# Performance work log

Hardware: AMD Instinct MI355X
Metric: run time of the kernel (lower is better)

The kernel has to match this reference:

```python
import jax, jax.numpy as jnp
import numpy as np

EMBED_DIM = 1024
NUM_HEADS = 16
HEAD_DIM = EMBED_DIM // NUM_HEADS

def setup_inputs() -> dict:
    key = jax.random.key(0)
    k1, k2, k3 = jax.random.split(key, 3)
    x = jax.random.normal(k1, (4, 2048, EMBED_DIM), dtype=jnp.float32)
    # Linear weights stored as [out, in] like torch; we apply x @ W.T
    W_qkv = jax.random.normal(k2, (3 * EMBED_DIM, EMBED_DIM), dtype=jnp.float32) * (EMBED_DIM ** -0.5)
    W_proj = jax.random.normal(k3, (EMBED_DIM, EMBED_DIM), dtype=jnp.float32) * (EMBED_DIM ** -0.5)
    return {"x": x, "W_qkv": W_qkv, "W_proj": W_proj}

def reference(x, W_qkv, W_proj):
    B, T, C = x.shape
    H, D = NUM_HEADS, HEAD_DIM
    qkv = x @ W_qkv.T                          # [B,T,3C]
    q, k, v = jnp.split(qkv, 3, axis=-1)
    q = q.reshape(B, T, H, D).transpose(0, 2, 1, 3)  # [B,H,T,D]
    k = k.reshape(B, T, H, D).transpose(0, 2, 1, 3)
    v = v.reshape(B, T, H, D).transpose(0, 2, 1, 3)
    scores = jnp.einsum('bhqd,bhkd->bhqk', q, k) / jnp.sqrt(jnp.asarray(D, x.dtype))
    causal = jnp.tril(jnp.ones((T, T), dtype=bool))
    scores = jnp.where(causal, scores, -jnp.inf)
    weights = jax.nn.softmax(scores, axis=-1)
    out = jnp.einsum('bhqk,bhkd->bhqd', weights, v)  # [B,H,T,D]
    out = out.transpose(0, 2, 1, 3).reshape(B, T, C)
    return out @ W_proj.T
```

## Files before the change

kernel.cpp:

```cpp
#include <hip/hip_runtime.h>

#define T_SEQ 2048
#define NB 4
#define NH 16
#define HD 64
#define CDIM 1024
#define MROWS (NB * T_SEQ)

typedef __attribute__((ext_vector_type(8))) short short8;
typedef __attribute__((ext_vector_type(4))) float floatx4;

static __device__ __forceinline__ unsigned short f2bf(float f) {
  union { float f; unsigned int i; } c; c.f = f;
  return (unsigned short)((c.i + 0x7FFFu + ((c.i >> 16) & 1u)) >> 16);
}
static __device__ __forceinline__ unsigned short f2bf_trunc(float f) {
  union { float f; unsigned int i; } c; c.f = f;
  return (unsigned short)(c.i >> 16);
}

static __device__ __forceinline__ void gl2lds16(const void* g, void* l) {
  __builtin_amdgcn_global_load_lds(
      (const __attribute__((address_space(1))) unsigned int*)g,
      (__attribute__((address_space(3))) unsigned int*)l, 16, 0, 0);
}

#define X4 (MROWS * CDIM / 4)
#define WQ4 (3 * CDIM * CDIM / 4)
#define WP4 (CDIM * CDIM / 4)
__global__ __launch_bounds__(256) void cast3_bf16(const float* __restrict__ x,
                                                  const float* __restrict__ wq,
                                                  const float* __restrict__ wp,
                                                  unsigned short* __restrict__ out) {
  const int i = blockIdx.x * 256 + threadIdx.x;
  const float* src; int off;
  if (i < X4) { src = x; off = i; }
  else if (i < X4 + WQ4) { src = wq; off = i - X4; }
  else { src = wp; off = i - X4 - WQ4; }
  const float4 v = ((const float4*)src)[off];
  ushort4 o;
  o.x = f2bf(v.x); o.y = f2bf(v.y); o.z = f2bf(v.z); o.w = f2bf(v.w);
  ((ushort4*)out)[i] = o;
}

#define Q_PRESCALE 0.18033688f

__global__ __launch_bounds__(256) void gemm_bf16_qkv(
    const unsigned short* __restrict__ A,
    const unsigned short* __restrict__ B,
    unsigned short* __restrict__ Oq,
    unsigned short* __restrict__ Ok,
    unsigned short* __restrict__ Ovt,
    const int K)
{
  __shared__ unsigned short As[128 * 32];
  __shared__ unsigned short Bs[128 * 32];
  const int tid = threadIdx.x;
  const int w = tid >> 6, l = tid & 63;
  const int quad = l >> 4, l15 = l & 15;
  const int m0 = blockIdx.y * 128, n0 = blockIdx.x * 128;
  const int wm = (w >> 1) * 64, wn = (w & 1) * 64;
  const int srow = l >> 2;
  const int scol = ((l & 3) ^ (srow & 3)) * 8;

  floatx4 acc[4][4];
#pragma unroll
  for (int mi = 0; mi < 4; ++mi)
#pragma unroll
    for (int ni = 0; ni < 4; ++ni) acc[mi][ni] = (floatx4){0.f, 0.f, 0.f, 0.f};

  const unsigned short* Ag = A + (size_t)(m0 + w * 32 + srow) * K + scol;
  const unsigned short* Bg = B + (size_t)(n0 + w * 32 + srow) * K + scol;
  unsigned short* Al0 = &As[(w * 32) * 32];
  unsigned short* Al1 = &As[(w * 32 + 16) * 32];
  unsigned short* Bl0 = &Bs[(w * 32) * 32];
  unsigned short* Bl1 = &Bs[(w * 32 + 16) * 32];
  const int sq = quad ^ (l15 & 3);

  for (int k0 = 0; k0 < K; k0 += 32) {
    __syncthreads();
    gl2lds16(Ag + k0, Al0);
    gl2lds16(Ag + (size_t)16 * K + k0, Al1);
    gl2lds16(Bg + k0, Bl0);
    gl2lds16(Bg + (size_t)16 * K + k0, Bl1);
    __syncthreads();
    short8 af[4], bfr[4];
#pragma unroll
    for (int mi = 0; mi < 4; ++mi)
      af[mi] = *(const short8*)&As[(wm + mi * 16 + l15) * 32 + sq * 8];
#pragma unroll
    for (int ni = 0; ni < 4; ++ni)
      bfr[ni] = *(const short8*)&Bs[(wn + ni * 16 + l15) * 32 + sq * 8];
#pragma unroll
    for (int mi = 0; mi < 4; ++mi)
#pragma unroll
      for (int ni = 0; ni < 4; ++ni)
        acc[mi][ni] = __builtin_amdgcn_mfma_f32_16x16x32_bf16(af[mi], bfr[ni], acc[mi][ni], 0, 0, 0);
  }

  const int mbase = m0 + wm + quad * 4;
#pragma unroll
  for (int ni = 0; ni < 4; ++ni) {
    const int n = n0 + wn + ni * 16 + l15;
    const int which = n >> 10;
    const int h = (n >> 6) & (NH - 1), d = n & (HD - 1);
    if (which == 2) {
#pragma unroll
      for (int mi = 0; mi < 4; ++mi) {
        const int m = mbase + mi * 16;
        const int b = m >> 11, t0 = m & (T_SEQ - 1);
        ushort4 pk;
        pk.x = f2bf(acc[mi][ni][0]); pk.y = f2bf(acc[mi][ni][1]);
        pk.z = f2bf(acc[mi][ni][2]); pk.w = f2bf(acc[mi][ni][3]);
        *(ushort4*)(Ovt + ((size_t)((b * NH + h) * HD + d) << 11) + t0) = pk;
      }
    } else {
      unsigned short* dst = (which == 0) ? Oq : Ok;
      const float sc = (which == 0) ? Q_PRESCALE : 1.0f;
#pragma unroll
      for (int mi = 0; mi < 4; ++mi)
#pragma unroll
        for (int r = 0; r < 4; ++r) {
          const int m = mbase + mi * 16 + r;
          const int b = m >> 11, t = m & (T_SEQ - 1);
          dst[(((size_t)(b * NH + h) * T_SEQ + t) << 6) + d] = f2bf(acc[mi][ni][r] * sc);
        }
    }
  }
}

__global__ __launch_bounds__(256) void gemm_bf16_proj(
    const unsigned short* __restrict__ A,
    const unsigned short* __restrict__ B,
    float* __restrict__ O,
    const int N, const int K)
{
  __shared__ unsigned short As[128 * 32];
  __shared__ unsigned short Bs[128 * 32];
  const int tid = threadIdx.x;
  const int w = tid >> 6, l = tid & 63;
  const int quad = l >> 4, l15 = l & 15;
  const int m0 = blockIdx.y * 128, n0 = blockIdx.x * 128;
  const int wm = (w >> 1) * 64, wn = (w & 1) * 64;
  const int srow = l >> 2;
  const int scol = ((l & 3) ^ (srow & 3)) * 8;

  floatx4 acc[4][4];
#pragma unroll
  for (int mi = 0; mi < 4; ++mi)
#pragma unroll
    for (int ni = 0; ni < 4; ++ni) acc[mi][ni] = (floatx4){0.f, 0.f, 0.f, 0.f};

  const unsigned short* Ag = A + (size_t)(m0 + w * 32 + srow) * K + scol;
  const unsigned short* Bg = B + (size_t)(n0 + w * 32 + srow) * K + scol;
  unsigned short* Al0 = &As[(w * 32) * 32];
  unsigned short* Al1 = &As[(w * 32 + 16) * 32];
  unsigned short* Bl0 = &Bs[(w * 32) * 32];
  unsigned short* Bl1 = &Bs[(w * 32 + 16) * 32];
  const int sq = quad ^ (l15 & 3);

  for (int k0 = 0; k0 < K; k0 += 32) {
    __syncthreads();
    gl2lds16(Ag + k0, Al0);
    gl2lds16(Ag + (size_t)16 * K + k0, Al1);
    gl2lds16(Bg + k0, Bl0);
    gl2lds16(Bg + (size_t)16 * K + k0, Bl1);
    __syncthreads();
    short8 af[4], bfr[4];
#pragma unroll
    for (int mi = 0; mi < 4; ++mi)
      af[mi] = *(const short8*)&As[(wm + mi * 16 + l15) * 32 + sq * 8];
#pragma unroll
    for (int ni = 0; ni < 4; ++ni)
      bfr[ni] = *(const short8*)&Bs[(wn + ni * 16 + l15) * 32 + sq * 8];
#pragma unroll
    for (int mi = 0; mi < 4; ++mi)
#pragma unroll
      for (int ni = 0; ni < 4; ++ni)
        acc[mi][ni] = __builtin_amdgcn_mfma_f32_16x16x32_bf16(af[mi], bfr[ni], acc[mi][ni], 0, 0, 0);
  }

#pragma unroll
  for (int mi = 0; mi < 4; ++mi)
#pragma unroll
    for (int r = 0; r < 4; ++r) {
      const int m = m0 + wm + mi * 16 + quad * 4 + r;
#pragma unroll
      for (int ni = 0; ni < 4; ++ni)
        O[(size_t)m * N + n0 + wn + ni * 16 + l15] = acc[mi][ni][r];
    }
}

#define TK 64

__global__ __launch_bounds__(512) void attn_mfma(
    const unsigned short* __restrict__ Q,
    const unsigned short* __restrict__ K,
    const unsigned short* __restrict__ Vt,
    unsigned short* __restrict__ O)
{
  __shared__ unsigned short Ks[TK * HD];
  __shared__ unsigned short Vts[HD * TK];
  __shared__ unsigned short Pw[8][16 * 68];
  const int tid = threadIdx.x;
  const int w = tid >> 6, l = tid & 63;
  const int quad = l >> 4, l15 = l & 15;
  const int drow = 8 * w + (l >> 3);
  const int dch = ((l & 7) ^ (l >> 3)) * 8;
  const int sw7 = l15 & 7;

  const int bh = blockIdx.x & 63;
  const int pp = blockIdx.x >> 6;
  const int b = bh >> 4, h = bh & 15;
  const size_t hoff = (size_t)bh * T_SEQ * HD;
  const unsigned short* Qh = Q + hoff;
  const unsigned short* Kdma = K + hoff + (size_t)drow * HD + dch;
  const unsigned short* Vdma = Vt + hoff + ((size_t)drow << 11) + dch;
  unsigned short* KsW = &Ks[w * 512];
  unsigned short* VtsW = &Vts[w * 512];

  short8 ones;
#pragma unroll
  for (int j = 0; j < 8; ++j) ones[j] = (short)0x3F80;

#pragma unroll 1
  for (int ii = 0; ii < 2; ++ii) {
    const int qtile = ii ? pp : (15 - pp);
    const int qw = qtile * 128 + w * 16;

    short8 qf[2];
    {
      const int qrow = qw + l15;
      qf[0] = *(const short8*)(Qh + (size_t)qrow * HD + quad * 8);
      qf[1] = *(const short8*)(Qh + (size_t)qrow * HD + 32 + quad * 8);
    }

    floatx4 Of[4];
#pragma unroll
    for (int dc = 0; dc < 4; ++dc) Of[dc] = (floatx4){0.f, 0.f, 0.f, 0.f};
    floatx4 lacc = (floatx4){0.f, 0.f, 0.f, 0.f};

    const int nkt = 2 * qtile + 2;
    for (int kt = 0; kt < nkt; ++kt) {
      const int kt0 = kt * TK;
      __syncthreads();
      gl2lds16(Kdma + (size_t)kt0 * HD, KsW);
      gl2lds16(Vdma + kt0, VtsW);
      __syncthreads();

      if (qw + 15 >= kt0) {
        floatx4 Sf[4];
#pragma unroll
        for (int cb = 0; cb < 4; ++cb) {
          Sf[cb] = (floatx4){0.f, 0.f, 0.f, 0.f};
          const int krow = cb * 16 + l15;
#pragma unroll
          for (int h2 = 0; h2 < 2; ++h2) {
            const int ch = (h2 * 4 + quad) ^ sw7;
            const short8 kf = *(const short8*)&Ks[krow * 64 + ch * 8];
            Sf[cb] = __builtin_amdgcn_mfma_f32_16x16x32_bf16(qf[h2], kf, Sf[cb], 0, 0, 0);
          }
        }
        const bool full = (kt0 + 63 <= qw);
        if (full) {
#pragma unroll
          for (int cb = 0; cb < 4; ++cb)
#pragma unroll
            for (int r = 0; r < 4; ++r)
              Pw[w][(quad * 4 + r) * 68 + cb * 16 + l15] = f2bf_trunc(exp2f(Sf[cb][r]));
        } else {
#pragma unroll
          for (int cb = 0; cb < 4; ++cb) {
            const int key = kt0 + cb * 16 + l15;
#pragma unroll
            for (int r = 0; r < 4; ++r) {
              const int qrow = qw + quad * 4 + r;
              const float p = (key > qrow) ? 0.f : exp2f(Sf[cb][r]);
              Pw[w][(quad * 4 + r) * 68 + cb * 16 + l15] = f2bf_trunc(p);
            }
          }
        }
#pragma unroll
        for (int kg = 0; kg < 2; ++kg) {
          const short8 pf = *(const short8*)&Pw[w][l15 * 68 + kg * 32 + quad * 8];
          lacc = __builtin_amdgcn_mfma_f32_16x16x32_bf16(pf, ones, lacc, 0, 0, 0);
#pragma unroll
          for (int dc = 0; dc < 4; ++dc) {
            const int vrow = dc * 16 + l15;
            const int ch = (kg * 4 + quad) ^ sw7;
            const short8 vf = *(const short8*)&Vts[vrow * 64 + ch * 8];
            Of[dc] = __builtin_amdgcn_mfma_f32_16x16x32_bf16(pf, vf, Of[dc], 0, 0, 0);
          }
        }
      }
    }

#pragma unroll
    for (int r = 0; r < 4; ++r) {
      const float inv = 1.f / lacc[r];
      const int q = qw + quad * 4 + r;
#pragma unroll
      for (int dc = 0; dc < 4; ++dc)
        O[(size_t)(b * T_SEQ + q) * CDIM + h * HD + dc * 16 + l15] = f2bf(Of[dc][r] * inv);
    }
  }
}

extern "C" void kernel_launch(void* const* d_in, const int* in_sizes, int n_in,
                              void* d_out, int out_size, void* d_ws, size_t ws_size,
                              hipStream_t stream) {
  const float* x     = (const float*)d_in[0];
  const float* Wqkv  = (const float*)d_in[1];
  const float* Wproj = (const float*)d_in[2];
  float* out = (float*)d_out;

  const size_t XSZ = (size_t)MROWS * CDIM;
  const size_t WQSZ = (size_t)3 * CDIM * CDIM;
  const size_t WPSZ = (size_t)CDIM * CDIM;
  unsigned short* xb  = (unsigned short*)d_ws;
  unsigned short* wqb = xb + XSZ;
  unsigned short* wpb = wqb + WQSZ;
  unsigned short* qbuf = wpb + WPSZ;
  unsigned short* kbuf = qbuf + XSZ;
  unsigned short* vtbuf = kbuf + XSZ;
  unsigned short* abuf = vtbuf + XSZ;

  cast3_bf16<<<(X4 + WQ4 + WP4) / 256, 256, 0, stream>>>(x, Wqkv, Wproj, xb);

  dim3 g1(3 * CDIM / 128, MROWS / 128);
  gemm_bf16_qkv<<<g1, 256, 0, stream>>>(xb, wqb, qbuf, kbuf, vtbuf, CDIM);

  attn_mfma<<<512, 512, 0, stream>>>(qbuf, kbuf, vtbuf, abuf);

  dim3 g3(CDIM / 128, MROWS / 128);
  gemm_bf16_proj<<<g3, 256, 0, stream>>>(abuf, wpb, out, CDIM, CDIM);
}
```

Before: 266.7 us.

## Double-buffer LDS tiles and transpose MFMA outputs for vectorized stores

All three kernels now double-buffer their LDS tiles. The next K or V tile is issued with global_load_lds before the current one is consumed, which drops one barrier per iteration and overlaps loads with MFMA work. MFMA operands are swapped so each lane's accumulator holds consecutive output columns. That allows packed ushort4/float4 stores for Q, K, attention output and projection output, and a transposed P layout in attention. The cost is twice the LDS per block, which may lower occupancy. The V-transpose store also becomes a scalar scatter.

```diff
diff --git a/kernel.cpp b/kernel.cpp
--- a/kernel.cpp
+++ b/kernel.cpp
@@ -53,8 +53,8 @@
     unsigned short* __restrict__ Ovt,
     const int K)
 {
-  __shared__ unsigned short As[128 * 32];
-  __shared__ unsigned short Bs[128 * 32];
+  __shared__ unsigned short As[2][128 * 32];
+  __shared__ unsigned short Bs[2][128 * 32];
   const int tid = threadIdx.x;
   const int w = tid >> 6, l = tid & 63;
   const int quad = l >> 4, l15 = l & 15;
@@ -71,60 +71,70 @@
 
   const unsigned short* Ag = A + (size_t)(m0 + w * 32 + srow) * K + scol;
   const unsigned short* Bg = B + (size_t)(n0 + w * 32 + srow) * K + scol;
-  unsigned short* Al0 = &As[(w * 32) * 32];
-  unsigned short* Al1 = &As[(w * 32 + 16) * 32];
-  unsigned short* Bl0 = &Bs[(w * 32) * 32];
-  unsigned short* Bl1 = &Bs[(w * 32 + 16) * 32];
+  const int d0 = (w * 32) * 32, d1 = (w * 32 + 16) * 32;
   const int sq = quad ^ (l15 & 3);
 
+  gl2lds16(Ag, &As[0][d0]);
+  gl2lds16(Ag + (size_t)16 * K, &As[0][d1]);
+  gl2lds16(Bg, &Bs[0][d0]);
+  gl2lds16(Bg + (size_t)16 * K, &Bs[0][d1]);
+
   for (int k0 = 0; k0 < K; k0 += 32) {
+    const int cur = (k0 >> 5) & 1, nxt = 1 - cur;
     __syncthreads();
-    gl2lds16(Ag + k0, Al0);
-    gl2lds16(Ag + (size_t)16 * K + k0, Al1);
-    gl2lds16(Bg + k0, Bl0);
-    gl2lds16(Bg + (size_t)16 * K + k0, Bl1);
-    __syncthreads();
+    if (k0 + 32 < K) {
+      gl2lds16(Ag + k0 + 32, &As[nxt][d0]);
+      gl2lds16(Ag + (size_t)16 * K + k0 + 32, &As[nxt][d1]);
+      gl2lds16(Bg + k0 + 32, &Bs[nxt][d0]);
+      gl2lds16(Bg + (size_t)16 * K + k0 + 32, &Bs[nxt][d1]);
+    }
     short8 af[4], bfr[4];
 #pragma unroll
     for (int mi = 0; mi < 4; ++mi)
-      af[mi] = *(const short8*)&As[(wm + mi * 16 + l15) * 32 + sq * 8];
+      af[mi] = *(const short8*)&As[cur][(wm + mi * 16 + l15) * 32 + sq * 8];
 #pragma unroll
     for (int ni = 0; ni < 4; ++ni)
-      bfr[ni] = *(const short8*)&Bs[(wn + ni * 16 + l15) * 32 + sq * 8];
+      bfr[ni] = *(const short8*)&Bs[cur][(wn + ni * 16 + l15) * 32 + sq * 8];
 #pragma unroll
     for (int mi = 0; mi < 4; ++mi)
 #pragma unroll
       for (int ni = 0; ni < 4; ++ni)
-        acc[mi][ni] = __builtin_amdgcn_mfma_f32_16x16x32_bf16(af[mi], bfr[ni], acc[mi][ni], 0, 0, 0);
-  }
-
-  const int mbase = m0 + wm + quad * 4;
-#pragma unroll
-  for (int ni = 0; ni < 4; ++ni) {
-    const int n = n0 + wn + ni * 16 + l15;
-    const int which = n >> 10;
-    const int h = (n >> 6) & (NH - 1), d = n & (HD - 1);
-    if (which == 2) {
+        acc[mi][ni] = __builtin_amdgcn_mfma_f32_16x16x32_bf16(bfr[ni], af[mi], acc[mi][ni], 0, 0, 0);
+  }
+
+  const int which = n0 >> 10;
+  if (which < 2) {
+    unsigned short* dst = (which == 0) ? Oq : Ok;
+    const float sc = (which == 0) ? Q_PRESCALE : 1.0f;
+#pragma unroll
+    for (int ni = 0; ni < 4; ++ni) {
+      const int n = n0 + wn + ni * 16 + quad * 4;
+      const int h = (n >> 6) & (NH - 1), d = n & (HD - 1);
 #pragma unroll
       for (int mi = 0; mi < 4; ++mi) {
-        const int m = mbase + mi * 16;
-        const int b = m >> 11, t0 = m & (T_SEQ - 1);
+        const int m = m0 + wm + mi * 16 + l15;
+        const int b = m >> 11, t = m & (T_SEQ - 1);
         ushort4 pk;
-        pk.x = f2bf(acc[mi][ni][0]); pk.y = f2bf(acc[mi][ni][1]);
-        pk.z = f2bf(acc[mi][ni][2]); pk.w = f2bf(acc[mi][ni][3]);
-        *(ushort4*)(Ovt + ((size_t)((b * NH + h) * HD + d) << 11) + t0) = pk;
+        pk.x = f2bf(acc[mi][ni][0] * sc); pk.y = f2bf(acc[mi][ni][1] * sc);
+        pk.z = f2bf(acc[mi][ni][2] * sc); pk.w = f2bf(acc[mi][ni][3] * sc);
+        *(ushort4*)(dst + (((size_t)(b * NH + h) * T_SEQ + t) << 6) + d) = pk;
       }
-    } else {
-      unsigned short* dst = (which == 0) ? Oq : Ok;
-      const float sc = (which == 0) ? Q_PRESCALE : 1.0f;
-#pragma unroll
-      for (int mi = 0; mi < 4; ++mi)
+    }
+  } else {
+#pragma unroll
+    for (int ni = 0; ni < 4; ++ni) {
+      const int nb = n0 + wn + ni * 16 + quad * 4;
+      const int h = (nb >> 6) & (NH - 1);
+#pragma unroll
+      for (int mi = 0; mi < 4; ++mi) {
+        const int m = m0 + wm + mi * 16 + l15;
+        const int b = m >> 11, t = m & (T_SEQ - 1);
 #pragma unroll
         for (int r = 0; r < 4; ++r) {
-          const int m = mbase + mi * 16 + r;
-          const int b = m >> 11, t = m & (T_SEQ - 1);
-          dst[(((size_t)(b * NH + h) * T_SEQ + t) << 6) + d] = f2bf(acc[mi][ni][r] * sc);
+          const int d = (nb + r) & (HD - 1);
+          Ovt[((size_t)((b * NH + h) * HD + d) << 11) + t] = f2bf(acc[mi][ni][r]);
         }
+      }
     }
   }
 }
@@ -135,8 +145,8 @@
     float* __restrict__ O,
     const int N, const int K)
 {
-  __shared__ unsigned short As[128 * 32];
-  __shared__ unsigned short Bs[128 * 32];
+  __shared__ unsigned short As[2][128 * 32];
+  __shared__ unsigned short Bs[2][128 * 32];
   const int tid = threadIdx.x;
   const int w = tid >> 6, l = tid & 63;
   const int quad = l >> 4, l15 = l & 15;
@@ -153,45 +163,51 @@
 
   const unsigned short* Ag = A + (size_t)(m0 + w * 32 + srow) * K + scol;
   const unsigned short* Bg = B + (size_t)(n0 + w * 32 + srow) * K + scol;
-  unsigned short* Al0 = &As[(w * 32) * 32];
-  unsigned short* Al1 = &As[(w * 32 + 16) * 32];
-  unsigned short* Bl0 = &Bs[(w * 32) * 32];
-  unsigned short* Bl1 = &Bs[(w * 32 + 16) * 32];
+  const int d0 = (w * 32) * 32, d1 = (w * 32 + 16) * 32;
   const int sq = quad ^ (l15 & 3);
 
+  gl2lds16(Ag, &As[0][d0]);
+  gl2lds16(Ag + (size_t)16 * K, &As[0][d1]);
+  gl2lds16(Bg, &Bs[0][d0]);
+  gl2lds16(Bg + (size_t)16 * K, &Bs[0][d1]);
+
   for (int k0 = 0; k0 < K; k0 += 32) {
+    const int cur = (k0 >> 5) & 1, nxt = 1 - cur;
     __syncthreads();
-    gl2lds16(Ag + k0, Al0);
-    gl2lds16(Ag + (size_t)16 * K + k0, Al1);
-    gl2lds16(Bg + k0, Bl0);
-    gl2lds16(Bg + (size_t)16 * K + k0, Bl1);
-    __syncthreads();
+    if (k0 + 32 < K) {
+      gl2lds16(Ag + k0 + 32, &As[nxt][d0]);
+      gl2lds16(Ag + (size_t)16 * K + k0 + 32, &As[nxt][d1]);
+      gl2lds16(Bg + k0 + 32, &Bs[nxt][d0]);
+      gl2lds16(Bg + (size_t)16 * K + k0 + 32, &Bs[nxt][d1]);
+    }
     short8 af[4], bfr[4];
 #pragma unroll
     for (int mi = 0; mi < 4; ++mi)
-      af[mi] = *(const short8*)&As[(wm + mi * 16 + l15) * 32 + sq * 8];
+      af[mi] = *(const short8*)&As[cur][(wm + mi * 16 + l15) * 32 + sq * 8];
 #pragma unroll
     for (int ni = 0; ni < 4; ++ni)
-      bfr[ni] = *(const short8*)&Bs[(wn + ni * 16 + l15) * 32 + sq * 8];
+      bfr[ni] = *(const short8*)&Bs[cur][(wn + ni * 16 + l15) * 32 + sq * 8];
 #pragma unroll
     for (int mi = 0; mi < 4; ++mi)
 #pragma unroll
       for (int ni = 0; ni < 4; ++ni)
-        acc[mi][ni] = __builtin_amdgcn_mfma_f32_16x16x32_bf16(af[mi], bfr[ni], acc[mi][ni], 0, 0, 0);
-  }
-
-#pragma unroll
-  for (int mi = 0; mi < 4; ++mi)
-#pragma unroll
-    for (int r = 0; r < 4; ++r) {
-      const int m = m0 + wm + mi * 16 + quad * 4 + r;
-#pragma unroll
-      for (int ni = 0; ni < 4; ++ni)
-        O[(size_t)m * N + n0 + wn + ni * 16 + l15] = acc[mi][ni][r];
-    }
+        acc[mi][ni] = __builtin_amdgcn_mfma_f32_16x16x32_bf16(bfr[ni], af[mi], acc[mi][ni], 0, 0, 0);
+  }
+
+#pragma unroll
+  for (int ni = 0; ni < 4; ++ni) {
+    const int n = n0 + wn + ni * 16 + quad * 4;
+#pragma unroll
+    for (int mi = 0; mi < 4; ++mi) {
+      const int m = m0 + wm + mi * 16 + l15;
+      *(float4*)(O + (size_t)m * N + n) =
+          make_float4(acc[mi][ni][0], acc[mi][ni][1], acc[mi][ni][2], acc[mi][ni][3]);
+    }
+  }
 }
 
 #define TK 64
+#define PTP 72
 
 __global__ __launch_bounds__(512) void attn_mfma(
     const unsigned short* __restrict__ Q,
@@ -199,9 +215,9 @@
     const unsigned short* __restrict__ Vt,
     unsigned short* __restrict__ O)
 {
-  __shared__ unsigned short Ks[TK * HD];
-  __shared__ unsigned short Vts[HD * TK];
-  __shared__ unsigned short Pw[8][16 * 68];
+  __shared__ unsigned short Ks[2][TK * HD];
+  __shared__ unsigned short Vts[2][HD * TK];
+  __shared__ unsigned short Pt[8][16 * PTP];
   const int tid = threadIdx.x;
   const int w = tid >> 6, l = tid & 63;
   const int quad = l >> 4, l15 = l & 15;
@@ -216,8 +232,7 @@
   const unsigned short* Qh = Q + hoff;
   const unsigned short* Kdma = K + hoff + (size_t)drow * HD + dch;
   const unsigned short* Vdma = Vt + hoff + ((size_t)drow << 11) + dch;
-  unsigned short* KsW = &Ks[w * 512];
-  unsigned short* VtsW = &Vts[w * 512];
+  const int wb = w * 512;
 
   short8 ones;
 #pragma unroll
@@ -241,12 +256,18 @@
     floatx4 lacc = (floatx4){0.f, 0.f, 0.f, 0.f};
 
     const int nkt = 2 * qtile + 2;
+    __syncthreads();
+    gl2lds16(Kdma, &Ks[0][wb]);
+    gl2lds16(Vdma, &Vts[0][wb]);
+
     for (int kt = 0; kt < nkt; ++kt) {
       const int kt0 = kt * TK;
+      const int cur = kt & 1, nxt = 1 - cur;
       __syncthreads();
-      gl2lds16(Kdma + (size_t)kt0 * HD, KsW);
-      gl2lds16(Vdma + kt0, VtsW);
-      __syncthreads();
+      if (kt + 1 < nkt) {
+        gl2lds16(Kdma + (size_t)(kt0 + TK) * HD, &Ks[nxt][wb]);
+        gl2lds16(Vdma + kt0 + TK, &Vts[nxt][wb]);
+      }
 
       if (qw + 15 >= kt0) {
         floatx4 Sf[4];
@@ -257,51 +278,53 @@
 #pragma unroll
           for (int h2 = 0; h2 < 2; ++h2) {
             const int ch = (h2 * 4 + quad) ^ sw7;
-            const short8 kf = *(const short8*)&Ks[krow * 64 + ch * 8];
-            Sf[cb] = __builtin_amdgcn_mfma_f32_16x16x32_bf16(qf[h2], kf, Sf[cb], 0, 0, 0);
+            const short8 kf = *(const short8*)&Ks[cur][krow * 64 + ch * 8];
+            Sf[cb] = __builtin_amdgcn_mfma_f32_16x16x32_bf16(kf, qf[h2], Sf[cb], 0, 0, 0);
           }
         }
         const bool full = (kt0 + 63 <= qw);
-        if (full) {
-#pragma unroll
-          for (int cb = 0; cb < 4; ++cb)
-#pragma unroll
-            for (int r = 0; r < 4; ++r)
-              Pw[w][(quad * 4 + r) * 68 + cb * 16 + l15] = f2bf_trunc(exp2f(Sf[cb][r]));
-        } else {
-#pragma unroll
-          for (int cb = 0; cb < 4; ++cb) {
-            const int key = kt0 + cb * 16 + l15;
-#pragma unroll
-            for (int r = 0; r < 4; ++r) {
-              const int qrow = qw + quad * 4 + r;
-              const float p = (key > qrow) ? 0.f : exp2f(Sf[cb][r]);
-              Pw[w][(quad * 4 + r) * 68 + cb * 16 + l15] = f2bf_trunc(p);
-            }
+        const int q = qw + l15;
+#pragma unroll
+        for (int cb = 0; cb < 4; ++cb) {
+          const int key0 = kt0 + cb * 16 + quad * 4;
+          ushort4 pk;
+          if (full) {
+            pk.x = f2bf_trunc(exp2f(Sf[cb][0]));
+            pk.y = f2bf_trunc(exp2f(Sf[cb][1]));
+            pk.z = f2bf_trunc(exp2f(Sf[cb][2]));
+            pk.w = f2bf_trunc(exp2f(Sf[cb][3]));
+          } else {
+            pk.x = (key0 + 0 > q) ? 0 : f2bf_trunc(exp2f(Sf[cb][0]));
+            pk.y = (key0 + 1 > q) ? 0 : f2bf_trunc(exp2f(Sf[cb][1]));
+            pk.z = (key0 + 2 > q) ? 0 : f2bf_trunc(exp2f(Sf[cb][2]));
+            pk.w = (key0 + 3 > q) ? 0 : f2bf_trunc(exp2f(Sf[cb][3]));
           }
+          *(ushort4*)&Pt[w][l15 * PTP + cb * 16 + quad * 4] = pk;
         }
 #pragma unroll
         for (int kg = 0; kg < 2; ++kg) {
-          const short8 pf = *(const short8*)&Pw[w][l15 * 68 + kg * 32 + quad * 8];
-          lacc = __builtin_amdgcn_mfma_f32_16x16x32_bf16(pf, ones, lacc, 0, 0, 0);
+          const short8 ptf = *(const short8*)&Pt[w][l15 * PTP + kg * 32 + quad * 8];
+          lacc = __builtin_amdgcn_mfma_f32_16x16x32_bf16(ones, ptf, lacc, 0, 0, 0);
 #pragma unroll
           for (int dc = 0; dc < 4; ++dc) {
             const int vrow = dc * 16 + l15;
             const int ch = (kg * 4 + quad) ^ sw7;
-            const short8 vf = *(const short8*)&Vts[vrow * 64 + ch * 8];
-            Of[dc] = __builtin_amdgcn_mfma_f32_16x16x32_bf16(pf, vf, Of[dc], 0, 0, 0);
+            const short8 vf = *(const short8*)&Vts[cur][vrow * 64 + ch * 8];
+            Of[dc] = __builtin_amdgcn_mfma_f32_16x16x32_bf16(vf, ptf, Of[dc], 0, 0, 0);
           }
         }
       }
     }
 
-#pragma unroll
-    for (int r = 0; r < 4; ++r) {
-      const float inv = 1.f / lacc[r];
-      const int q = qw + quad * 4 + r;
-#pragma unroll
-      for (int dc = 0; dc < 4; ++dc)
-        O[(size_t)(b * T_SEQ + q) * CDIM + h * HD + dc * 16 + l15] = f2bf(Of[dc][r] * inv);
+    const float inv = 1.f / lacc[0];
+    const int q = qw + l15;
+    unsigned short* orow = O + (size_t)(b * T_SEQ + q) * CDIM + h * HD + quad * 4;
+#pragma unroll
+    for (int dc = 0; dc < 4; ++dc) {
+      ushort4 ov;
+      ov.x = f2bf(Of[dc][0] * inv); ov.y = f2bf(Of[dc][1] * inv);
+      ov.z = f2bf(Of[dc][2] * inv); ov.w = f2bf(Of[dc][3] * inv);
+      *(ushort4*)(orow + dc * 16) = ov;
     }
   }
 }
```

Measured after the change: 250.5 us. -6.1%, faster.
